# Performance work log

Measured on AMD Instinct MI355X. Metric: run time of the kernel, lower is better.

The kernel has to match this reference:

```python
import jax, jax.numpy as jnp
import numpy as np

B, WORDS, DIM = 16, 32, 256
HEADS, DIM_HEAD = 8, 32
INNER = HEADS * DIM_HEAD  # 256 == DIM -> project_out True
ITER = 3
J = WORDS * HEADS  # input capsules axis


def setup_inputs() -> dict:
    key = jax.random.key(0)
    ks = jax.random.split(key, 6)
    x = jax.random.normal(ks[0], (B, WORDS, DIM), jnp.float32)
    # capsule transform weights: [J, I, E, D] = [words*heads, words, inner, dim_head]
    W = jax.random.normal(ks[1], (J, WORDS, INNER, DIM_HEAD), jnp.float32)
    bias = 0.01 * jax.random.normal(ks[2], (J, WORDS, INNER), jnp.float32)
    Wi = jax.random.normal(ks[3], (INNER, DIM), jnp.float32) / np.sqrt(DIM)
    bi = jnp.zeros((INNER,), jnp.float32)
    Wo = jax.random.normal(ks[4], (DIM, INNER), jnp.float32) / np.sqrt(INNER)
    bo = jnp.zeros((DIM,), jnp.float32)
    return {"x": x, "W": W, "bias": bias, "Wi": Wi, "bi": bi, "Wo": Wo, "bo": bo}


def _squash(s):
    n = jnp.linalg.norm(s, axis=-1, keepdims=True)
    return n / (1.0 + n * n) * s


def reference(x, W, bias, Wi, bi, Wo, bo):
    # inner projection: [B, WORDS, INNER]
    xi = x @ Wi.T + bi
    # 'b n (h d) -> b (n h) d'
    xh = xi.reshape(B, WORDS * HEADS, DIM_HEAD)
    # u_hat[b,j,i,e] = sum_d W[j,i,e,d] * xh[b,j,d]  -> [B, J, WORDS, INNER]
    u_hat = jnp.einsum('jied,bjd->bjie', W, xh) + bias
    u_det = jax.lax.stop_gradient(u_hat)
    b_log = jnp.zeros_like(u_hat)
    v = None
    for i in range(ITER):
        c = jax.nn.softmax(b_log, axis=2)          # over output capsules (words)
        u = u_hat if i == ITER - 1 else u_det       # detach except last iter
        s = jnp.sum(c * u, axis=1, keepdims=True)   # [B,1,WORDS,INNER]
        v = _squash(s)
        if i < ITER - 1:
            b_log = b_log + jnp.sum(u_det * v, axis=3, keepdims=True)
    out = jnp.squeeze(v, 1) @ Wo.T + bo             # [B, WORDS, DIM]
    return out
```

## Files before the change

kernel.cpp:

```cpp
#include <hip/hip_runtime.h>

#define BB   16
#define NW   32
#define DIMM 256
#define DH   32
#define NI   256
#define NJ   256
#define JP   4
#define JG   (NJ / JP)

__global__ void k_proj_in(const float* __restrict__ x, const float* __restrict__ Wi,
                          const float* __restrict__ bi, float* __restrict__ xh) {
    int row = blockIdx.x;
    int k = threadIdx.x;
    __shared__ float xr[DIMM];
    xr[k] = x[(size_t)row * DIMM + k];
    __syncthreads();
    const float4* wi  = (const float4*)(Wi + (size_t)k * DIMM);
    const float4* xr4 = (const float4*)xr;
    float acc = bi[k];
#pragma unroll 8
    for (int m = 0; m < DIMM / 4; ++m) {
        float4 w = wi[m]; float4 xv = xr4[m];
        acc += w.x * xv.x + w.y * xv.y + w.z * xv.z + w.w * xv.w;
    }
    xh[(size_t)row * DIMM + k] = acc;
}

__global__ void k_uhat(const float* __restrict__ W, const float* __restrict__ bias,
                       const float* __restrict__ xh, float* __restrict__ u,
                       float* __restrict__ part) {
    int jg = blockIdx.x >> 5;
    int i  = blockIdx.x & 31;
    int e  = threadIdx.x;
    const size_t BSTR = (size_t)NJ * NW * NI;
    float acc0[BB];
#pragma unroll
    for (int b = 0; b < BB; ++b) acc0[b] = 0.f;

    for (int jj = 0; jj < JP; ++jj) {
        int j = jg * JP + jj;
        const float4* wp = (const float4*)(W + (((size_t)j * NW + i) * NI + e) * DH);
        float4 w4[8];
#pragma unroll
        for (int q = 0; q < 8; ++q) w4[q] = wp[q];
        const float* w = (const float*)w4;
        float bv = bias[((size_t)j * NW + i) * NI + e];
        float* up = u + ((size_t)j * NW + i) * NI + e;
#pragma unroll
        for (int b = 0; b < BB; ++b) {
            const float* xb = xh + ((size_t)b * NJ + j) * DH;
            float a = bv;
#pragma unroll
            for (int d = 0; d < DH; ++d) a += w[d] * xb[d];
            up[(size_t)b * BSTR] = a;
            acc0[b] += a;
        }
    }
#pragma unroll
    for (int b = 0; b < BB; ++b)
        part[(((size_t)b * JG + jg) * NW + i) * NI + e] = acc0[b];
}

__global__ void __launch_bounds__(256, 4)
k_route(const float* __restrict__ u, const float* __restrict__ v,
        float* __restrict__ b_log, float* __restrict__ part, int accflag) {
    int b  = blockIdx.x / JG;
    int jg = blockIdx.x % JG;
    int t  = threadIdx.x;
    int i  = t >> 3;
    int h  = t & 7;
    __shared__ float sh_beta[JP][NW];

    float vr[32];
    {
        const float4* vp = (const float4*)(v + ((size_t)b * NW + i) * NI + h * 32);
#pragma unroll
        for (int q = 0; q < 8; ++q) ((float4*)vr)[q] = vp[q];
    }
    float s_acc[32];
#pragma unroll
    for (int k = 0; k < 32; ++k) s_acc[k] = 0.f;

    for (int jj = 0; jj < JP; ++jj) {
        int j = jg * JP + jj;
        float ur[32];
        {
            const float4* up = (const float4*)(u + (((size_t)b * NJ + j) * NW + i) * NI + h * 32);
#pragma unroll
            for (int q = 0; q < 8; ++q) ((float4*)ur)[q] = up[q];
        }
        float p = 0.f;
#pragma unroll
        for (int k = 0; k < 32; ++k) p += ur[k] * vr[k];
        p += __shfl_xor(p, 1);
        p += __shfl_xor(p, 2);
        p += __shfl_xor(p, 4);
        if (h == 0) {
            size_t bidx = ((size_t)b * NJ + j) * NW + i;
            float bta = p;
            if (accflag) bta += b_log[bidx];
            b_log[bidx] = bta;
            sh_beta[jj][i] = bta;
        }
        __syncthreads();
        float r0 = sh_beta[jj][h * 4 + 0];
        float r1 = sh_beta[jj][h * 4 + 1];
        float r2 = sh_beta[jj][h * 4 + 2];
        float r3 = sh_beta[jj][h * 4 + 3];
        float m = fmaxf(fmaxf(r0, r1), fmaxf(r2, r3));
        m = fmaxf(m, __shfl_xor(m, 1));
        m = fmaxf(m, __shfl_xor(m, 2));
        m = fmaxf(m, __shfl_xor(m, 4));
        float ss = __expf(r0 - m) + __expf(r1 - m) + __expf(r2 - m) + __expf(r3 - m);
        ss += __shfl_xor(ss, 1);
        ss += __shfl_xor(ss, 2);
        ss += __shfl_xor(ss, 4);
        float c = __expf(sh_beta[jj][i] - m) / ss;
#pragma unroll
        for (int k = 0; k < 32; ++k) s_acc[k] += c * ur[k];
    }
    float4* pp = (float4*)(part + (((size_t)b * JG + jg) * NW + i) * NI + h * 32);
#pragma unroll
    for (int q = 0; q < 8; ++q) pp[q] = ((float4*)s_acc)[q];
}

__global__ void k_reduce(const float* __restrict__ part, float* __restrict__ v,
                         float scale) {
    int b = blockIdx.x >> 5;
    int i = blockIdx.x & 31;
    int tid = threadIdx.x;
    int lane = tid & 63, wave = tid >> 6;
    float acc = 0.f;
#pragma unroll 16
    for (int g = 0; g < JG; ++g)
        acc += part[(((size_t)b * JG + g) * NW + i) * NI + tid];
    acc *= scale;
    __shared__ float red[4];
    float p = acc * acc;
#pragma unroll
    for (int off = 32; off >= 1; off >>= 1) p += __shfl_down(p, off);
    if (lane == 0) red[wave] = p;
    __syncthreads();
    float n2 = red[0] + red[1] + red[2] + red[3];
    float n = sqrtf(n2);
    float f = n / (1.0f + n2);
    v[((size_t)b * NW + i) * NI + tid] = f * acc;
}

__global__ void k_proj_out(const float* __restrict__ v, const float* __restrict__ Wo,
                           const float* __restrict__ bo, float* __restrict__ out) {
    int row = blockIdx.x;
    int k = threadIdx.x;
    __shared__ float vr[NI];
    vr[k] = v[(size_t)row * NI + k];
    __syncthreads();
    const float4* wo  = (const float4*)(Wo + (size_t)k * NI);
    const float4* vr4 = (const float4*)vr;
    float acc = bo[k];
#pragma unroll 8
    for (int m = 0; m < NI / 4; ++m) {
        float4 w = wo[m]; float4 xv = vr4[m];
        acc += w.x * xv.x + w.y * xv.y + w.z * xv.z + w.w * xv.w;
    }
    out[(size_t)row * DIMM + k] = acc;
}

extern "C" void kernel_launch(void* const* d_in, const int* in_sizes, int n_in,
                              void* d_out, int out_size, void* d_ws, size_t ws_size,
                              hipStream_t stream) {
    const float* x    = (const float*)d_in[0];
    const float* W    = (const float*)d_in[1];
    const float* bias = (const float*)d_in[2];
    const float* Wi   = (const float*)d_in[3];
    const float* bi   = (const float*)d_in[4];
    const float* Wo   = (const float*)d_in[5];
    const float* bo   = (const float*)d_in[6];
    float* out = (float*)d_out;

    float* ws    = (float*)d_ws;
    float* xh    = ws;
    float* u     = ws + 131072;
    float* part  = u + 33554432;
    float* b_log = part + 8388608;
    float* v     = b_log + 131072;

    k_proj_in<<<dim3(BB * NW), dim3(256), 0, stream>>>(x, Wi, bi, xh);
    k_uhat<<<dim3(JG * NW), dim3(256), 0, stream>>>(W, bias, xh, u, part);
    k_reduce<<<dim3(BB * NW), dim3(256), 0, stream>>>(part, v, 1.0f / NW);
    k_route<<<dim3(BB * JG), dim3(256), 0, stream>>>(u, v, b_log, part, 0);
    k_reduce<<<dim3(BB * NW), dim3(256), 0, stream>>>(part, v, 1.0f);
    k_route<<<dim3(BB * JG), dim3(256), 0, stream>>>(u, v, b_log, part, 1);
    k_reduce<<<dim3(BB * NW), dim3(256), 0, stream>>>(part, v, 1.0f);
    k_proj_out<<<dim3(BB * NW), dim3(256), 0, stream>>>(v, Wo, bo, out);
}
```

Measured before the change: 574.6 us.

## Fuse all routing stages into one cooperative persistent kernel with grid syncs

Replaces the eight separate kernel launches with a single cooperative kernel of 1024 blocks that runs each stage in a grid-stride loop, separated by grid-wide barriers. This removes per-launch overhead and the gaps between kernels. The u_hat stage now stages the xh slice in shared memory instead of reading it from global memory per thread. The fused kernel adds grid-sync cost and needs all 1024 blocks resident at once; if the cooperative launch fails, the original multi-kernel path runs instead.

```diff
diff --git a/kernel.cpp b/kernel.cpp
--- a/kernel.cpp
+++ b/kernel.cpp
@@ -1,4 +1,7 @@
 #include <hip/hip_runtime.h>
+#include <hip/hip_cooperative_groups.h>
+
+namespace cg = cooperative_groups;
 
 #define BB   16
 #define NW   32
@@ -8,6 +11,192 @@
 #define NJ   256
 #define JP   4
 #define JG   (NJ / JP)
+#define GRID 1024
+
+
+__device__ __forceinline__ void phase_reduce(const float* __restrict__ part,
+                                             float* __restrict__ v, float scale,
+                                             int nb, int bid, int tid, float* sm) {
+    for (int unit = bid; unit < BB * NW; unit += nb) {
+        int b = unit >> 5, i = unit & 31;
+        int lane = tid & 63, wave = tid >> 6;
+        float acc = 0.f;
+#pragma unroll 16
+        for (int g = 0; g < JG; ++g)
+            acc += part[(((size_t)b * JG + g) * NW + i) * NI + tid];
+        acc *= scale;
+        float p = acc * acc;
+#pragma unroll
+        for (int off = 32; off >= 1; off >>= 1) p += __shfl_down(p, off);
+        __syncthreads();
+        if (lane == 0) sm[wave] = p;
+        __syncthreads();
+        float n2 = sm[0] + sm[1] + sm[2] + sm[3];
+        float n = sqrtf(n2);
+        float f = n / (1.0f + n2);
+        v[((size_t)b * NW + i) * NI + tid] = f * acc;
+    }
+}
+
+__device__ __forceinline__ void phase_route(const float* __restrict__ u,
+                                            const float* __restrict__ v,
+                                            float* __restrict__ b_log,
+                                            float* __restrict__ part, int accflag,
+                                            int nb, int bid, int tid, float* sm) {
+    for (int unit = bid; unit < BB * JG; unit += nb) {
+        int b = unit / JG, jg = unit % JG;
+        int i = tid >> 3, h = tid & 7;
+        float vr[32];
+        {
+            const float4* vp = (const float4*)(v + ((size_t)b * NW + i) * NI + h * 32);
+#pragma unroll
+            for (int q = 0; q < 8; ++q) ((float4*)vr)[q] = vp[q];
+        }
+        float s_acc[32];
+#pragma unroll
+        for (int k = 0; k < 32; ++k) s_acc[k] = 0.f;
+
+        for (int jj = 0; jj < JP; ++jj) {
+            int j = jg * JP + jj;
+            float ur[32];
+            {
+                const float4* up = (const float4*)(u + (((size_t)b * NJ + j) * NW + i) * NI + h * 32);
+#pragma unroll
+                for (int q = 0; q < 8; ++q) ((float4*)ur)[q] = up[q];
+            }
+            float p = 0.f;
+#pragma unroll
+            for (int k = 0; k < 32; ++k) p += ur[k] * vr[k];
+            p += __shfl_xor(p, 1);
+            p += __shfl_xor(p, 2);
+            p += __shfl_xor(p, 4);
+            __syncthreads();
+            if (h == 0) {
+                size_t bidx = ((size_t)b * NJ + j) * NW + i;
+                float bta = p;
+                if (accflag) bta += b_log[bidx];
+                b_log[bidx] = bta;
+                sm[i] = bta;
+            }
+            __syncthreads();
+            float r0 = sm[h * 4 + 0];
+            float r1 = sm[h * 4 + 1];
+            float r2 = sm[h * 4 + 2];
+            float r3 = sm[h * 4 + 3];
+            float m = fmaxf(fmaxf(r0, r1), fmaxf(r2, r3));
+            m = fmaxf(m, __shfl_xor(m, 1));
+            m = fmaxf(m, __shfl_xor(m, 2));
+            m = fmaxf(m, __shfl_xor(m, 4));
+            float ss = __expf(r0 - m) + __expf(r1 - m) + __expf(r2 - m) + __expf(r3 - m);
+            ss += __shfl_xor(ss, 1);
+            ss += __shfl_xor(ss, 2);
+            ss += __shfl_xor(ss, 4);
+            float c = __expf(sm[i] - m) / ss;
+#pragma unroll
+            for (int k = 0; k < 32; ++k) s_acc[k] += c * ur[k];
+        }
+        float4* pp = (float4*)(part + (((size_t)b * JG + jg) * NW + i) * NI + h * 32);
+#pragma unroll
+        for (int q = 0; q < 8; ++q) pp[q] = ((float4*)s_acc)[q];
+    }
+}
+
+__global__ void __launch_bounds__(256, 4)
+k_fused(const float* __restrict__ x, const float* __restrict__ W,
+        const float* __restrict__ bias, const float* __restrict__ Wi,
+        const float* __restrict__ bi, const float* __restrict__ Wo,
+        const float* __restrict__ bo, float* __restrict__ out,
+        float* __restrict__ xh, float* __restrict__ u,
+        float* __restrict__ part, float* __restrict__ b_log,
+        float* __restrict__ v) {
+    cg::grid_group gg = cg::this_grid();
+    const int bid = blockIdx.x;
+    const int tid = threadIdx.x;
+    const int nb = gridDim.x;
+    __shared__ float sm[JP * BB * DH];
+
+    for (int row = bid; row < BB * NW; row += nb) {
+        __syncthreads();
+        sm[tid] = x[(size_t)row * DIMM + tid];
+        __syncthreads();
+        const float4* wi  = (const float4*)(Wi + (size_t)tid * DIMM);
+        const float4* xr4 = (const float4*)sm;
+        float acc = bi[tid];
+#pragma unroll 8
+        for (int m = 0; m < DIMM / 4; ++m) {
+            float4 w = wi[m]; float4 xv = xr4[m];
+            acc += w.x * xv.x + w.y * xv.y + w.z * xv.z + w.w * xv.w;
+        }
+        xh[(size_t)row * DIMM + tid] = acc;
+    }
+    gg.sync();
+
+    for (int unit = bid; unit < JG * NW; unit += nb) {
+        int jg = unit >> 5;
+        int i  = unit & 31;
+        int e  = tid;
+        __syncthreads();
+        for (int t = tid; t < JP * BB * DH; t += 256) {
+            int jj = t >> 9;
+            int rem = t & 511;
+            int b = rem >> 5, d = rem & 31;
+            sm[t] = xh[((size_t)b * NJ + jg * JP + jj) * DH + d];
+        }
+        __syncthreads();
+        float acc0[BB];
+#pragma unroll
+        for (int b = 0; b < BB; ++b) acc0[b] = 0.f;
+        for (int jj = 0; jj < JP; ++jj) {
+            int j = jg * JP + jj;
+            const float4* wp = (const float4*)(W + (((size_t)j * NW + i) * NI + e) * DH);
+            float4 w4[8];
+#pragma unroll
+            for (int q = 0; q < 8; ++q) w4[q] = wp[q];
+            const float* w = (const float*)w4;
+            float bv = bias[((size_t)j * NW + i) * NI + e];
+            const float* xs = sm + jj * (BB * DH);
+#pragma unroll
+            for (int b = 0; b < BB; ++b) {
+                float a = bv;
+#pragma unroll
+                for (int d = 0; d < DH; ++d) a += w[d] * xs[b * 32 + d];
+                u[(((size_t)b * NJ + j) * NW + i) * NI + e] = a;
+                acc0[b] += a;
+            }
+        }
+#pragma unroll
+        for (int b = 0; b < BB; ++b)
+            part[(((size_t)b * JG + jg) * NW + i) * NI + e] = acc0[b];
+    }
+    gg.sync();
+
+    phase_reduce(part, v, 1.0f / NW, nb, bid, tid, sm);
+    gg.sync();
+    phase_route(u, v, b_log, part, 0, nb, bid, tid, sm);
+    gg.sync();
+    phase_reduce(part, v, 1.0f, nb, bid, tid, sm);
+    gg.sync();
+    phase_route(u, v, b_log, part, 1, nb, bid, tid, sm);
+    gg.sync();
+    phase_reduce(part, v, 1.0f, nb, bid, tid, sm);
+    gg.sync();
+
+    for (int row = bid; row < BB * NW; row += nb) {
+        __syncthreads();
+        sm[tid] = v[(size_t)row * NI + tid];
+        __syncthreads();
+        const float4* wo  = (const float4*)(Wo + (size_t)tid * NI);
+        const float4* vr4 = (const float4*)sm;
+        float acc = bo[tid];
+#pragma unroll 8
+        for (int m = 0; m < NI / 4; ++m) {
+            float4 w = wo[m]; float4 xv = vr4[m];
+            acc += w.x * xv.x + w.y * xv.y + w.z * xv.z + w.w * xv.w;
+        }
+        out[(size_t)row * DIMM + tid] = acc;
+    }
+}
+
 
 __global__ void k_proj_in(const float* __restrict__ x, const float* __restrict__ Wi,
                           const float* __restrict__ bi, float* __restrict__ xh) {
@@ -33,11 +222,17 @@
     int jg = blockIdx.x >> 5;
     int i  = blockIdx.x & 31;
     int e  = threadIdx.x;
-    const size_t BSTR = (size_t)NJ * NW * NI;
+    __shared__ float xs[JP * BB * DH];
+    for (int t = threadIdx.x; t < JP * BB * DH; t += 256) {
+        int jj = t >> 9;
+        int rem = t & 511;
+        int b = rem >> 5, d = rem & 31;
+        xs[t] = xh[((size_t)b * NJ + jg * JP + jj) * DH + d];
+    }
+    __syncthreads();
     float acc0[BB];
 #pragma unroll
     for (int b = 0; b < BB; ++b) acc0[b] = 0.f;
-
     for (int jj = 0; jj < JP; ++jj) {
         int j = jg * JP + jj;
         const float4* wp = (const float4*)(W + (((size_t)j * NW + i) * NI + e) * DH);
@@ -46,14 +241,13 @@
         for (int q = 0; q < 8; ++q) w4[q] = wp[q];
         const float* w = (const float*)w4;
         float bv = bias[((size_t)j * NW + i) * NI + e];
-        float* up = u + ((size_t)j * NW + i) * NI + e;
+        const float* xp = xs + jj * (BB * DH);
 #pragma unroll
         for (int b = 0; b < BB; ++b) {
-            const float* xb = xh + ((size_t)b * NJ + j) * DH;
             float a = bv;
 #pragma unroll
-            for (int d = 0; d < DH; ++d) a += w[d] * xb[d];
-            up[(size_t)b * BSTR] = a;
+            for (int d = 0; d < DH; ++d) a += w[d] * xp[b * 32 + d];
+            u[(((size_t)b * NJ + j) * NW + i) * NI + e] = a;
             acc0[b] += a;
         }
     }
@@ -65,13 +259,12 @@
 __global__ void __launch_bounds__(256, 4)
 k_route(const float* __restrict__ u, const float* __restrict__ v,
         float* __restrict__ b_log, float* __restrict__ part, int accflag) {
+    __shared__ float sm[NW];
     int b  = blockIdx.x / JG;
     int jg = blockIdx.x % JG;
     int t  = threadIdx.x;
     int i  = t >> 3;
     int h  = t & 7;
-    __shared__ float sh_beta[JP][NW];
-
     float vr[32];
     {
         const float4* vp = (const float4*)(v + ((size_t)b * NW + i) * NI + h * 32);
@@ -81,7 +274,6 @@
     float s_acc[32];
 #pragma unroll
     for (int k = 0; k < 32; ++k) s_acc[k] = 0.f;
-
     for (int jj = 0; jj < JP; ++jj) {
         int j = jg * JP + jj;
         float ur[32];
@@ -96,18 +288,19 @@
         p += __shfl_xor(p, 1);
         p += __shfl_xor(p, 2);
         p += __shfl_xor(p, 4);
+        __syncthreads();
         if (h == 0) {
             size_t bidx = ((size_t)b * NJ + j) * NW + i;
             float bta = p;
             if (accflag) bta += b_log[bidx];
             b_log[bidx] = bta;
-            sh_beta[jj][i] = bta;
-        }
-        __syncthreads();
-        float r0 = sh_beta[jj][h * 4 + 0];
-        float r1 = sh_beta[jj][h * 4 + 1];
-        float r2 = sh_beta[jj][h * 4 + 2];
-        float r3 = sh_beta[jj][h * 4 + 3];
+            sm[i] = bta;
+        }
+        __syncthreads();
+        float r0 = sm[h * 4 + 0];
+        float r1 = sm[h * 4 + 1];
+        float r2 = sm[h * 4 + 2];
+        float r3 = sm[h * 4 + 3];
         float m = fmaxf(fmaxf(r0, r1), fmaxf(r2, r3));
         m = fmaxf(m, __shfl_xor(m, 1));
         m = fmaxf(m, __shfl_xor(m, 2));
@@ -116,7 +309,7 @@
         ss += __shfl_xor(ss, 1);
         ss += __shfl_xor(ss, 2);
         ss += __shfl_xor(ss, 4);
-        float c = __expf(sh_beta[jj][i] - m) / ss;
+        float c = __expf(sm[i] - m) / ss;
 #pragma unroll
         for (int k = 0; k < 32; ++k) s_acc[k] += c * ur[k];
     }
@@ -185,12 +378,19 @@
     float* b_log = part + 8388608;
     float* v     = b_log + 131072;
 
-    k_proj_in<<<dim3(BB * NW), dim3(256), 0, stream>>>(x, Wi, bi, xh);
-    k_uhat<<<dim3(JG * NW), dim3(256), 0, stream>>>(W, bias, xh, u, part);
-    k_reduce<<<dim3(BB * NW), dim3(256), 0, stream>>>(part, v, 1.0f / NW);
-    k_route<<<dim3(BB * JG), dim3(256), 0, stream>>>(u, v, b_log, part, 0);
-    k_reduce<<<dim3(BB * NW), dim3(256), 0, stream>>>(part, v, 1.0f);
-    k_route<<<dim3(BB * JG), dim3(256), 0, stream>>>(u, v, b_log, part, 1);
-    k_reduce<<<dim3(BB * NW), dim3(256), 0, stream>>>(part, v, 1.0f);
-    k_proj_out<<<dim3(BB * NW), dim3(256), 0, stream>>>(v, Wo, bo, out);
-}
+    void* args[] = {(void*)&x, (void*)&W, (void*)&bias, (void*)&Wi, (void*)&bi,
+                    (void*)&Wo, (void*)&bo, (void*)&out, (void*)&xh, (void*)&u,
+                    (void*)&part, (void*)&b_log, (void*)&v};
+    hipError_t err = hipLaunchCooperativeKernel((const void*)k_fused, dim3(GRID),
+                                                dim3(256), args, 0, stream);
+    if (err != hipSuccess) {
+        k_proj_in<<<dim3(BB * NW), dim3(256), 0, stream>>>(x, Wi, bi, xh);
+        k_uhat<<<dim3(JG * NW), dim3(256), 0, stream>>>(W, bias, xh, u, part);
+        k_reduce<<<dim3(BB * NW), dim3(256), 0, stream>>>(part, v, 1.0f / NW);
+        k_route<<<dim3(BB * JG), dim3(256), 0, stream>>>(u, v, b_log, part, 0);
+        k_reduce<<<dim3(BB * NW), dim3(256), 0, stream>>>(part, v, 1.0f);
+        k_route<<<dim3(BB * JG), dim3(256), 0, stream>>>(u, v, b_log, part, 1);
+        k_reduce<<<dim3(BB * NW), dim3(256), 0, stream>>>(part, v, 1.0f);
+        k_proj_out<<<dim3(BB * NW), dim3(256), 0, stream>>>(v, Wo, bo, out);
+    }
+}
```

After: 1.539 ms. 168% more time.

## Replace partial-sum buffers and reduce kernels with atomic accumulation and fused squash

Applied to the files above, without the earlier changes.

Removes the separate k_reduce kernels and the large partial-sum buffer. The uhat and route kernels now atomically add their per-group sums straight into small s buffers, which proj_in zeroes. The squash step is recomputed inside each consumer: route applies it to its input s, and proj_out applies it before the output projection. Groups per block rise from 4 to 8 to cut the number of atomics, at the cost of fewer blocks, a lower occupancy hint, an extra barrier per loop step, and non-deterministic float summation order.

```diff
diff --git a/kernel.cpp b/kernel.cpp
--- a/kernel.cpp
+++ b/kernel.cpp
@@ -6,13 +6,19 @@
 #define DH   32
 #define NI   256
 #define NJ   256
-#define JP   4
-#define JG   (NJ / JP)
+#define JPU  8
+#define JGU  (NJ / JPU)
+#define JPR  8
+#define JGR  (NJ / JPR)
 
 __global__ void k_proj_in(const float* __restrict__ x, const float* __restrict__ Wi,
-                          const float* __restrict__ bi, float* __restrict__ xh) {
+                          const float* __restrict__ bi, float* __restrict__ xh,
+                          float* __restrict__ s0, float* __restrict__ s1,
+                          float* __restrict__ s2) {
     int row = blockIdx.x;
     int k = threadIdx.x;
+    size_t idx = (size_t)row * 256 + k;
+    s0[idx] = 0.f; s1[idx] = 0.f; s2[idx] = 0.f;
     __shared__ float xr[DIMM];
     xr[k] = x[(size_t)row * DIMM + k];
     __syncthreads();
@@ -29,17 +35,16 @@
 
 __global__ void k_uhat(const float* __restrict__ W, const float* __restrict__ bias,
                        const float* __restrict__ xh, float* __restrict__ u,
-                       float* __restrict__ part) {
+                       float* __restrict__ s0) {
     int jg = blockIdx.x >> 5;
     int i  = blockIdx.x & 31;
     int e  = threadIdx.x;
-    const size_t BSTR = (size_t)NJ * NW * NI;
     float acc0[BB];
 #pragma unroll
     for (int b = 0; b < BB; ++b) acc0[b] = 0.f;
 
-    for (int jj = 0; jj < JP; ++jj) {
-        int j = jg * JP + jj;
+    for (int jj = 0; jj < JPU; ++jj) {
+        int j = jg * JPU + jj;
         const float4* wp = (const float4*)(W + (((size_t)j * NW + i) * NI + e) * DH);
         float4 w4[8];
 #pragma unroll
@@ -53,37 +58,50 @@
             float a = bv;
 #pragma unroll
             for (int d = 0; d < DH; ++d) a += w[d] * xb[d];
-            up[(size_t)b * BSTR] = a;
+            up[(size_t)b * NJ * NW * NI] = a;
             acc0[b] += a;
         }
     }
 #pragma unroll
     for (int b = 0; b < BB; ++b)
-        part[(((size_t)b * JG + jg) * NW + i) * NI + e] = acc0[b];
-}
-
-__global__ void __launch_bounds__(256, 4)
-k_route(const float* __restrict__ u, const float* __restrict__ v,
-        float* __restrict__ b_log, float* __restrict__ part, int accflag) {
-    int b  = blockIdx.x / JG;
-    int jg = blockIdx.x % JG;
+        atomicAdd(&s0[((size_t)b * NW + i) * NI + e], acc0[b]);
+}
+
+__global__ void __launch_bounds__(256, 2)
+k_route(const float* __restrict__ u, const float* __restrict__ s_in,
+        float* __restrict__ b_log, float* __restrict__ s_out,
+        float vscale, int accflag) {
+    int b  = blockIdx.x >> 5;
+    int jg = blockIdx.x & 31;
     int t  = threadIdx.x;
     int i  = t >> 3;
     int h  = t & 7;
-    __shared__ float sh_beta[JP][NW];
+    __shared__ float sm[NW];
 
     float vr[32];
     {
-        const float4* vp = (const float4*)(v + ((size_t)b * NW + i) * NI + h * 32);
-#pragma unroll
-        for (int q = 0; q < 8; ++q) ((float4*)vr)[q] = vp[q];
-    }
+        const float4* sp = (const float4*)(s_in + ((size_t)b * NW + i) * NI + h * 32);
+#pragma unroll
+        for (int q = 0; q < 8; ++q) ((float4*)vr)[q] = sp[q];
+    }
+    float n2p = 0.f;
+#pragma unroll
+    for (int k = 0; k < 32; ++k) n2p += vr[k] * vr[k];
+    n2p += __shfl_xor(n2p, 1);
+    n2p += __shfl_xor(n2p, 2);
+    n2p += __shfl_xor(n2p, 4);
+    float n2 = vscale * vscale * n2p;
+    float n  = sqrtf(n2);
+    float f  = n / (1.0f + n2) * vscale;
+#pragma unroll
+    for (int k = 0; k < 32; ++k) vr[k] *= f;
+
     float s_acc[32];
 #pragma unroll
     for (int k = 0; k < 32; ++k) s_acc[k] = 0.f;
 
-    for (int jj = 0; jj < JP; ++jj) {
-        int j = jg * JP + jj;
+    for (int jj = 0; jj < JPR; ++jj) {
+        int j = jg * JPR + jj;
         float ur[32];
         {
             const float4* up = (const float4*)(u + (((size_t)b * NJ + j) * NW + i) * NI + h * 32);
@@ -96,18 +114,19 @@
         p += __shfl_xor(p, 1);
         p += __shfl_xor(p, 2);
         p += __shfl_xor(p, 4);
+        __syncthreads();
         if (h == 0) {
             size_t bidx = ((size_t)b * NJ + j) * NW + i;
             float bta = p;
             if (accflag) bta += b_log[bidx];
             b_log[bidx] = bta;
-            sh_beta[jj][i] = bta;
+            sm[i] = bta;
         }
         __syncthreads();
-        float r0 = sh_beta[jj][h * 4 + 0];
-        float r1 = sh_beta[jj][h * 4 + 1];
-        float r2 = sh_beta[jj][h * 4 + 2];
-        float r3 = sh_beta[jj][h * 4 + 3];
+        float r0 = sm[h * 4 + 0];
+        float r1 = sm[h * 4 + 1];
+        float r2 = sm[h * 4 + 2];
+        float r3 = sm[h * 4 + 3];
         float m = fmaxf(fmaxf(r0, r1), fmaxf(r2, r3));
         m = fmaxf(m, __shfl_xor(m, 1));
         m = fmaxf(m, __shfl_xor(m, 2));
@@ -116,28 +135,24 @@
         ss += __shfl_xor(ss, 1);
         ss += __shfl_xor(ss, 2);
         ss += __shfl_xor(ss, 4);
-        float c = __expf(sh_beta[jj][i] - m) / ss;
+        float c = __expf(sm[i] - m) / ss;
 #pragma unroll
         for (int k = 0; k < 32; ++k) s_acc[k] += c * ur[k];
     }
-    float4* pp = (float4*)(part + (((size_t)b * JG + jg) * NW + i) * NI + h * 32);
-#pragma unroll
-    for (int q = 0; q < 8; ++q) pp[q] = ((float4*)s_acc)[q];
-}
-
-__global__ void k_reduce(const float* __restrict__ part, float* __restrict__ v,
-                         float scale) {
-    int b = blockIdx.x >> 5;
-    int i = blockIdx.x & 31;
-    int tid = threadIdx.x;
-    int lane = tid & 63, wave = tid >> 6;
-    float acc = 0.f;
-#pragma unroll 16
-    for (int g = 0; g < JG; ++g)
-        acc += part[(((size_t)b * JG + g) * NW + i) * NI + tid];
-    acc *= scale;
+    float* so = s_out + ((size_t)b * NW + i) * NI + h * 32;
+#pragma unroll
+    for (int k = 0; k < 32; ++k) atomicAdd(&so[k], s_acc[k]);
+}
+
+__global__ void k_proj_out(const float* __restrict__ s2, const float* __restrict__ Wo,
+                           const float* __restrict__ bo, float* __restrict__ out) {
+    int row = blockIdx.x;
+    int k = threadIdx.x;
+    int lane = k & 63, wave = k >> 6;
+    __shared__ float vrow[NI];
     __shared__ float red[4];
-    float p = acc * acc;
+    float sv = s2[(size_t)row * NI + k];
+    float p = sv * sv;
 #pragma unroll
     for (int off = 32; off >= 1; off >>= 1) p += __shfl_down(p, off);
     if (lane == 0) red[wave] = p;
@@ -145,18 +160,10 @@
     float n2 = red[0] + red[1] + red[2] + red[3];
     float n = sqrtf(n2);
     float f = n / (1.0f + n2);
-    v[((size_t)b * NW + i) * NI + tid] = f * acc;
-}
-
-__global__ void k_proj_out(const float* __restrict__ v, const float* __restrict__ Wo,
-                           const float* __restrict__ bo, float* __restrict__ out) {
-    int row = blockIdx.x;
-    int k = threadIdx.x;
-    __shared__ float vr[NI];
-    vr[k] = v[(size_t)row * NI + k];
+    vrow[k] = f * sv;
     __syncthreads();
     const float4* wo  = (const float4*)(Wo + (size_t)k * NI);
-    const float4* vr4 = (const float4*)vr;
+    const float4* vr4 = (const float4*)vrow;
     float acc = bo[k];
 #pragma unroll 8
     for (int m = 0; m < NI / 4; ++m) {
@@ -181,16 +188,14 @@
     float* ws    = (float*)d_ws;
     float* xh    = ws;
     float* u     = ws + 131072;
-    float* part  = u + 33554432;
-    float* b_log = part + 8388608;
-    float* v     = b_log + 131072;
-
-    k_proj_in<<<dim3(BB * NW), dim3(256), 0, stream>>>(x, Wi, bi, xh);
-    k_uhat<<<dim3(JG * NW), dim3(256), 0, stream>>>(W, bias, xh, u, part);
-    k_reduce<<<dim3(BB * NW), dim3(256), 0, stream>>>(part, v, 1.0f / NW);
-    k_route<<<dim3(BB * JG), dim3(256), 0, stream>>>(u, v, b_log, part, 0);
-    k_reduce<<<dim3(BB * NW), dim3(256), 0, stream>>>(part, v, 1.0f);
-    k_route<<<dim3(BB * JG), dim3(256), 0, stream>>>(u, v, b_log, part, 1);
-    k_reduce<<<dim3(BB * NW), dim3(256), 0, stream>>>(part, v, 1.0f);
-    k_proj_out<<<dim3(BB * NW), dim3(256), 0, stream>>>(v, Wo, bo, out);
-}
+    float* b_log = u + 33554432;
+    float* s0    = b_log + 131072;
+    float* s1    = s0 + 131072;
+    float* s2    = s1 + 131072;
+
+    k_proj_in<<<dim3(BB * NW), dim3(256), 0, stream>>>(x, Wi, bi, xh, s0, s1, s2);
+    k_uhat<<<dim3(JGU * NW), dim3(256), 0, stream>>>(W, bias, xh, u, s0);
+    k_route<<<dim3(BB * JGR), dim3(256), 0, stream>>>(u, s0, b_log, s1, 1.0f / NW, 0);
+    k_route<<<dim3(BB * JGR), dim3(256), 0, stream>>>(u, s1, b_log, s2, 1.0f, 1);
+    k_proj_out<<<dim3(BB * NW), dim3(256), 0, stream>>>(s2, Wo, bo, out);
+}
```

After: 893.9 us. 55.6% more time.
